# Kernel optimization log

Hardware: AMD Instinct MI355X
Metric: run time of the kernel (lower is better)

Reference implementation:

```python
import jax, jax.numpy as jnp
import numpy as np

N, E = 50000, 800000          # nodes, edges (self-loops added in reference)
IN_C, HID, OUT_C = 512, 128, 40
K, H = 4, 8                   # n_layers, heads
C = HID // H                  # per-head channels = 16
L = K + 1                     # with_initial_residual=True -> K+1 convs
NEG_SLOPE = 0.2               # PyG GATConv default leaky_relu slope


def setup_inputs():
    key = jax.random.key(0)
    ks = jax.random.split(key, 12)
    s = 0.05
    x = jax.random.normal(ks[0], (N, IN_C), jnp.float32)
    edge_index = jax.random.randint(ks[1], (2, E), 0, N, dtype=jnp.int32)
    fc0_w = jax.random.normal(ks[2], (IN_C, HID), jnp.float32) * s
    fc0_b = jax.random.normal(ks[3], (HID,), jnp.float32) * s
    lin_w = jax.random.normal(ks[4], (L, HID, HID), jnp.float32) * s      # GATConv lin (bias=False)
    att_src = jax.random.normal(ks[5], (L, H, C), jnp.float32) * s
    att_dst = jax.random.normal(ks[6], (L, H, C), jnp.float32) * s
    conv_bias = jax.random.normal(ks[7], (L, HID), jnp.float32) * s
    alphas = jnp.zeros((L,), jnp.float32).at[0].set(1.0)                  # init_alphas: t[0]=1
    fc1_w = jax.random.normal(ks[8], (HID, OUT_C), jnp.float32) * s
    fc1_b = jax.random.normal(ks[9], (OUT_C,), jnp.float32) * s
    return {"x": x, "edge_index": edge_index, "fc0_w": fc0_w, "fc0_b": fc0_b,
            "lin_w": lin_w, "att_src": att_src, "att_dst": att_dst,
            "conv_bias": conv_bias, "alphas": alphas, "fc1_w": fc1_w, "fc1_b": fc1_b}


def _gat_conv(h, src, dst, lin_w, a_src_w, a_dst_w, bias):
    # PyG GATConv (eval mode): linear -> edgewise attention -> segment softmax -> scatter-sum
    hp = (h @ lin_w).reshape(N, H, C)                 # [N,H,C]
    a_src = jnp.einsum('nhc,hc->nh', hp, a_src_w)     # [N,H]
    a_dst = jnp.einsum('nhc,hc->nh', hp, a_dst_w)
    e = jax.nn.leaky_relu(a_src[src] + a_dst[dst], NEG_SLOPE)   # [E+N,H]
    emax = jax.ops.segment_max(e, dst, num_segments=N)          # per-dst, per-head max
    e = jnp.exp(e - emax[dst])
    denom = jax.ops.segment_sum(e, dst, num_segments=N)
    alpha = e / (denom[dst] + 1e-16)                            # segment softmax
    msg = hp[src] * alpha[:, :, None]                           # [E+N,H,C]
    out = jax.ops.segment_sum(msg, dst, num_segments=N)         # [N,H,C]
    return out.reshape(N, H * C) + bias


def reference(x, edge_index, fc0_w, fc0_b, lin_w, att_src, att_dst, conv_bias, alphas, fc1_w, fc1_b):
    # forward_clenshawRes, eval mode (dropout = identity, batchNorm=False)
    loops = jnp.arange(N, dtype=edge_index.dtype)
    src = jnp.concatenate([edge_index[0], loops])   # add self-loops (PyG default)
    dst = jnp.concatenate([edge_index[1], loops])
    h0 = x @ fc0_w + fc0_b                          # fcs[0]
    last = jnp.zeros_like(h0)
    second_last = jnp.zeros_like(h0)
    for i in range(L):
        hcur = jax.nn.elu(_gat_conv(last, src, dst, lin_w[i], att_src[i], att_dst[i], conv_bias[i]))
        hcur = 2.0 * hcur - second_last + alphas[L - 1 - i] * h0   # alphas[-(i+1)]
        second_last, last = last, hcur
    out = last @ fc1_w + fc1_b                      # fcs[-1]
    return jax.nn.log_softmax(out, axis=1)
```

## Files before the change

### kernel.cpp

```cpp
#include <hip/hip_runtime.h>
#include <math.h>

#define NN      50000
#define E_CNT   800000
#define IN_C    512
#define HID     128
#define OUT_C   40
#define NHEAD   8
#define CPH     16
#define NLAYER  5
#define NEG     0.2f
#define CAP     64
#define NCOL    144

typedef __attribute__((ext_vector_type(8))) short bf16x8;
typedef __attribute__((ext_vector_type(4))) float f32x4;

__device__ __forceinline__ float lrelu(float x) { return x > 0.f ? x : NEG * x; }
__device__ __forceinline__ float eluf(float x)  { return x > 0.f ? x : expm1f(x); }

__device__ __forceinline__ float bf2f(unsigned short u) {
    union { unsigned int a; float f; } v; v.a = ((unsigned int)u) << 16;
    return v.f;
}
__device__ __forceinline__ float2 bf2f2(unsigned int u) {
    union { unsigned int a; float f; } lo, hi;
    lo.a = u << 16; hi.a = u & 0xffff0000u;
    return make_float2(lo.f, hi.f);
}
__device__ __forceinline__ unsigned short f2bf(float f) {
    union { float f; unsigned int u; } v; v.f = f;
    return (unsigned short)((v.u + 0x7fffu + ((v.u >> 16) & 1u)) >> 16);
}
__device__ __forceinline__ unsigned int pack2(float a, float b) {
    return ((unsigned int)f2bf(b) << 16) | f2bf(a);
}

__device__ __forceinline__ void gl2lds16(const void* g, void* l) {
    __builtin_amdgcn_global_load_lds(
        (const __attribute__((address_space(1))) unsigned int*)g,
        (__attribute__((address_space(3))) unsigned int*)l, 16, 0, 0);
}

__global__ __launch_bounds__(256) void k_wt(const float* __restrict__ w,
                                            unsigned short* __restrict__ wt, int K, int opitch) {
    __shared__ float t[32][33];
    const float* ws = w + (size_t)blockIdx.z * K * HID;
    unsigned short* wd = wt + (size_t)blockIdx.z * opitch;
    int k0 = blockIdx.x * 32, n0 = blockIdx.y * 32;
    int tx = threadIdx.x & 31, ty = threadIdx.x >> 5;
    for (int r = ty; r < 32; r += 8) t[r][tx] = ws[(size_t)(k0 + r) * HID + n0 + tx];
    __syncthreads();
    for (int r = ty; r < 32; r += 8) wd[(size_t)(n0 + r) * K + k0 + tx] = f2bf(t[tx][r]);
}

__global__ void k_watt(const float* __restrict__ linw, const float* __restrict__ attS,
                       const float* __restrict__ attD, unsigned short* __restrict__ wt2) {
    int i = blockIdx.x * blockDim.x + threadIdx.x;
    if (i >= 4 * 16 * HID) return;
    int l = i >> 11, r = (i >> 7) & 15, k = i & 127;
    int h = r & 7, isD = r >> 3;
    const float* W = linw + (size_t)(l + 1) * HID * HID;
    const float* av = (isD ? attD : attS) + (size_t)(l + 1) * NHEAD * CPH + h * CPH;
    float s = 0.f;
#pragma unroll
    for (int c = 0; c < CPH; ++c) s += W[(size_t)k * HID + h * CPH + c] * av[c];
    wt2[(size_t)l * NCOL * HID + (size_t)(128 + r) * HID + k] = f2bf(s);
}

template<int K, int A_F32, int NT, int EPI>
__global__ __launch_bounds__(256) void k_mgemm(const void* __restrict__ aptr,
                                               const unsigned short* __restrict__ wt,
                                               const float* __restrict__ bias,
                                               const float* __restrict__ cb0,
                                               const float* __restrict__ alphas,
                                               unsigned short* __restrict__ out_b,
                                               unsigned short* __restrict__ out_h0,
                                               float* __restrict__ aSo,
                                               float* __restrict__ aDo) {
    __shared__ unsigned short As[64 * 32];
    __shared__ unsigned short Bs[NT * 16 * 32];
    const int tid  = threadIdx.x;
    const int w    = tid >> 6, lane = tid & 63;
    const int fr   = lane & 15, fq = lane >> 4;
    const int row0 = blockIdx.x * 64;
    const int rowb = row0 + w * 16;
    const int rs = lane >> 2;
    const int ko = (lane & 3) * 8;
    f32x4 acc[NT] = {};

    for (int k0 = 0; k0 < K; k0 += 32) {
        if (A_F32) {
            int row = tid >> 2, kb = (tid & 3) * 8;
            int grow = row0 + row; if (grow >= NN) grow = NN - 1;
            const float* s = (const float*)aptr + (size_t)grow * K + k0 + kb;
            float4 v0 = *(const float4*)s, v1 = *(const float4*)(s + 4);
            union { bf16x8 v; unsigned int u[4]; } pk;
            pk.u[0] = pack2(v0.x, v0.y); pk.u[1] = pack2(v0.z, v0.w);
            pk.u[2] = pack2(v1.x, v1.y); pk.u[3] = pack2(v1.z, v1.w);
            *(bf16x8*)&As[row * 32 + kb] = pk.v;
            for (int j = w; j < NT; j += 4)
                gl2lds16(wt + (size_t)(j * 16 + rs) * K + k0 + ko, &Bs[j * 16 * 32]);
        } else {
            for (int c = w; c < 4 + NT; c += 4) {
                if (c < 4) {
                    int grow = row0 + c * 16 + rs; if (grow >= NN) grow = NN - 1;
                    gl2lds16((const unsigned short*)aptr + (size_t)grow * K + k0 + ko,
                             &As[c * 16 * 32]);
                } else {
                    int j = c - 4;
                    gl2lds16(wt + (size_t)(j * 16 + rs) * K + k0 + ko, &Bs[j * 16 * 32]);
                }
            }
        }
        __syncthreads();
        bf16x8 af = *(const bf16x8*)&As[(w * 16 + fr) * 32 + fq * 8];
#pragma unroll
        for (int t = 0; t < NT; ++t) {
            bf16x8 bfr = *(const bf16x8*)&Bs[(t * 16 + fr) * 32 + fq * 8];
            acc[t] = __builtin_amdgcn_mfma_f32_16x16x32_bf16(af, bfr, acc[t], 0, 0, 0);
        }
        __syncthreads();
    }

    const int cl = lane & 15, rq = (lane >> 4) * 4;
    const float a4 = (EPI == 2) ? alphas[NLAYER - 1] : 0.f;
#pragma unroll
    for (int t = 0; t < 8; ++t) {
        int col = t * 16 + cl;
        float bcol = (EPI == 2) ? bias[col] : 0.f;
        float ecol = (EPI == 2) ? 2.f * eluf(cb0[col]) : 0.f;
#pragma unroll
        for (int rg = 0; rg < 4; ++rg) {
            int row = rowb + rq + rg;
            if (row < NN) {
                if (EPI == 0) {
                    out_b[(size_t)row * HID + col] = f2bf(acc[t][rg]);
                } else {
                    float h0v = acc[t][rg] + bcol;
                    out_h0[(size_t)row * HID + col] = f2bf(h0v);
                    out_b[(size_t)row * HID + col]  = f2bf(ecol + a4 * h0v);
                }
            }
        }
    }
    if (NT == 9) {
#pragma unroll
        for (int rg = 0; rg < 4; ++rg) {
            int row = rowb + rq + rg;
            if (row < NN) {
                float v = acc[8][rg];
                if (cl < 8) aSo[(size_t)row * NHEAD + cl] = v;
                else        aDo[(size_t)row * NHEAD + (cl - 8)] = v;
            }
        }
    }
}

__global__ void k_hist(const int* __restrict__ dst, int* __restrict__ deg) {
    int e = blockIdx.x * blockDim.x + threadIdx.x;
    if (e < E_CNT) atomicAdd(&deg[dst[e]], 1);
}

__global__ __launch_bounds__(1024) void k_part(const int* __restrict__ deg, int* __restrict__ part) {
    int i = blockIdx.x * 1024 + threadIdx.x;
    int v = (i < NN) ? deg[i] : 0;
    for (int off = 32; off; off >>= 1) v += __shfl_down(v, off);
    __shared__ int ws[16];
    if ((threadIdx.x & 63) == 0) ws[threadIdx.x >> 6] = v;
    __syncthreads();
    if (threadIdx.x < 16) {
        int t = ws[threadIdx.x];
        for (int off = 8; off; off >>= 1) t += __shfl_down(t, off);
        if (threadIdx.x == 0) part[blockIdx.x] = t;
    }
}

__global__ void k_scanpart(int* __restrict__ part, int* __restrict__ rowstart, int nb) {
    int t = threadIdx.x;
    int v = (t < nb) ? part[t] : 0;
    int x = v;
    for (int off = 1; off < 64; off <<= 1) { int u = __shfl_up(x, off); if (t >= off) x += u; }
    if (t < nb) part[t] = x - v;
    if (t == nb - 1) rowstart[NN] = x;
}

__global__ __launch_bounds__(1024) void k_scanblk(const int* __restrict__ deg,
                                                  const int* __restrict__ partx,
                                                  int* __restrict__ rowstart,
                                                  int* __restrict__ cursor) {
    int b = blockIdx.x, t = threadIdx.x, i = b * 1024 + t;
    int v = (i < NN) ? deg[i] : 0;
    int x = v;
    for (int off = 1; off < 64; off <<= 1) { int u = __shfl_up(x, off); if ((t & 63) >= off) x += u; }
    __shared__ int ws[16];
    if ((t & 63) == 63) ws[t >> 6] = x;
    __syncthreads();
    if (t < 64) {
        int wv = (t < 16) ? ws[t] : 0;
        for (int off = 1; off < 16; off <<= 1) { int u = __shfl_up(wv, off); if (t >= off) wv += u; }
        if (t < 16) ws[t] = wv;
    }
    __syncthreads();
    int waveoff = (t >= 64) ? ws[(t >> 6) - 1] : 0;
    int excl = x - v + waveoff + partx[b];
    if (i < NN) { rowstart[i] = excl; cursor[i] = excl; }
}

__global__ void k_scatter(const int* __restrict__ src, const int* __restrict__ dst,
                          int* __restrict__ cursor, int* __restrict__ csr) {
    int e = blockIdx.x * blockDim.x + threadIdx.x;
    if (e < E_CNT) {
        int p = atomicAdd(&cursor[dst[e]], 1);
        csr[p] = src[e];
    }
}

__global__ __launch_bounds__(256) void k_agg(
    const unsigned short* __restrict__ hpb, const float* __restrict__ aS, const float* __restrict__ aD,
    const int* __restrict__ rowstart, const int* __restrict__ csr,
    const float* __restrict__ bias, const unsigned short* __restrict__ h0b,
    const unsigned short* __restrict__ slb, const float* __restrict__ alphas, int aidx, int sl_zero,
    unsigned int* __restrict__ outb) {
    __shared__ int   slds[4][CAP];
    __shared__ float wlds[4][CAP][NHEAD];
    const int wave = threadIdx.x >> 6;
    const int lane = threadIdx.x & 63;
    const int n    = blockIdx.x * 4 + wave;
    const int rsb  = rowstart[n];
    const int deg  = rowstart[n + 1] - rsb;
    const int cnt  = deg < CAP ? deg : CAP;

    for (int j = lane; j < cnt; j += 64) slds[wave][j] = csr[rsb + j];
    __syncthreads();

    const int h    = lane & 7;
    const int slot = lane >> 3;
    const float adst = aD[n * NHEAD + h];

    float den = 0.f;
#pragma unroll
    for (int t = 0; t < 8; ++t) {
        int j = slot + t * 8;
        if (j < cnt) {
            int s = slds[wave][j];
            float wv = __expf(lrelu(aS[s * NHEAD + h] + adst));
            wlds[wave][j][h] = wv;
            den += wv;
        }
    }
    for (int j = CAP + slot; j < deg; j += 8)
        den += __expf(lrelu(aS[csr[rsb + j] * NHEAD + h] + adst));
#pragma unroll
    for (int off = 8; off < 64; off <<= 1) den += __shfl_xor(den, off);
    const float w0 = __expf(lrelu(aS[n * NHEAD + h] + adst));
    den += w0;
    const float dinv = 1.f / (den + 1e-16f);
    __syncthreads();

    const int l    = lane & 31;
    const int half = lane >> 5;
    const int hh   = l >> 2;
    const float w0h = __shfl(w0, hh);
    const float dih = __shfl(dinv, hh);
    const float adh = __shfl(adst, hh);

    float a0 = 0.f, a1 = 0.f, a2 = 0.f, a3 = 0.f;
    if (half == 0) {
        uint2 u = *(const uint2*)(hpb + (size_t)n * HID + 4 * l);
        float2 p = bf2f2(u.x), q = bf2f2(u.y);
        a0 = w0h * p.x; a1 = w0h * p.y; a2 = w0h * q.x; a3 = w0h * q.y;
    }
    if (deg <= CAP) {
#pragma unroll 4
        for (int j = half; j < deg; j += 2) {
            int s = slds[wave][j];
            float wv = wlds[wave][j][hh];
            uint2 u = *(const uint2*)(hpb + (size_t)s * HID + 4 * l);
            float2 p = bf2f2(u.x), q = bf2f2(u.y);
            a0 += wv * p.x; a1 += wv * p.y; a2 += wv * q.x; a3 += wv * q.y;
        }
    } else {
        for (int j = half; j < deg; j += 2) {
            int s; float wv;
            if (j < CAP) { s = slds[wave][j]; wv = wlds[wave][j][hh]; }
            else { s = csr[rsb + j]; wv = __expf(lrelu(aS[s * NHEAD + hh] + adh)); }
            uint2 u = *(const uint2*)(hpb + (size_t)s * HID + 4 * l);
            float2 p = bf2f2(u.x), q = bf2f2(u.y);
            a0 += wv * p.x; a1 += wv * p.y; a2 += wv * q.x; a3 += wv * q.y;
        }
    }
    a0 += __shfl_xor(a0, 32); a1 += __shfl_xor(a1, 32);
    a2 += __shfl_xor(a2, 32); a3 += __shfl_xor(a3, 32);

    if (half == 0) {
        float4 bv = ((const float4*)bias)[l];
        float g0 = eluf(a0 * dih + bv.x);
        float g1 = eluf(a1 * dih + bv.y);
        float g2 = eluf(a2 * dih + bv.z);
        float g3 = eluf(a3 * dih + bv.w);
        const float ac = alphas[aidx];
        float s0 = 0.f, s1 = 0.f, s2 = 0.f, s3 = 0.f;
        if (!sl_zero) {
            uint2 su = *(const uint2*)(slb + (size_t)n * HID + 4 * l);
            float2 p = bf2f2(su.x), q = bf2f2(su.y);
            s0 = p.x; s1 = p.y; s2 = q.x; s3 = q.y;
        }
        float hx0 = 0.f, hx1 = 0.f, hx2 = 0.f, hx3 = 0.f;
        if (ac != 0.f) {
            uint2 hu = *(const uint2*)(h0b + (size_t)n * HID + 4 * l);
            float2 p = bf2f2(hu.x), q = bf2f2(hu.y);
            hx0 = p.x; hx1 = p.y; hx2 = q.x; hx3 = q.y;
        }
        float o0 = 2.f * g0 - s0 + ac * hx0;
        float o1 = 2.f * g1 - s1 + ac * hx1;
        float o2 = 2.f * g2 - s2 + ac * hx2;
        float o3 = 2.f * g3 - s3 + ac * hx3;
        uint2 pb; pb.x = pack2(o0, o1); pb.y = pack2(o2, o3);
        ((uint2*)outb)[(size_t)n * 32 + l] = pb;
    }
}

__global__ __launch_bounds__(64) void k_out(const unsigned short* __restrict__ t,
                                            const float* __restrict__ w,
                                            const float* __restrict__ b,
                                            float* __restrict__ out) {
    const int n = blockIdx.x;
    const int lane = threadIdx.x;
    float acc = 0.f;
    if (lane < OUT_C) {
        const unsigned short* row = t + (size_t)n * HID;
        for (int k = 0; k < HID; ++k) acc += bf2f(row[k]) * w[k * OUT_C + lane];
        acc += b[lane];
    }
    float v = (lane < OUT_C) ? acc : -INFINITY;
    for (int off = 32; off; off >>= 1) v = fmaxf(v, __shfl_down(v, off));
    float mx = __shfl(v, 0);
    float ex = (lane < OUT_C) ? __expf(acc - mx) : 0.f;
    float sv = ex;
    for (int off = 32; off; off >>= 1) sv += __shfl_down(sv, off);
    float lse = logf(__shfl(sv, 0));
    if (lane < OUT_C) out[(size_t)n * OUT_C + lane] = acc - mx - lse;
}

extern "C" void kernel_launch(void* const* d_in, const int* in_sizes, int n_in,
                              void* d_out, int out_size, void* d_ws, size_t ws_size,
                              hipStream_t stream) {
    const float* x      = (const float*)d_in[0];
    const int*   ei     = (const int*)  d_in[1];
    const float* fc0w   = (const float*)d_in[2];
    const float* fc0b   = (const float*)d_in[3];
    const float* linw   = (const float*)d_in[4];
    const float* attS   = (const float*)d_in[5];
    const float* attD   = (const float*)d_in[6];
    const float* cbias  = (const float*)d_in[7];
    const float* alphas = (const float*)d_in[8];
    const float* fc1w   = (const float*)d_in[9];
    const float* fc1b   = (const float*)d_in[10];
    float* out = (float*)d_out;

    char* p = (char*)d_ws;
    auto alloc = [&](size_t bytes) { void* q = (void*)p; p += (bytes + 255) / 256 * 256; return q; };
    const size_t NB16 = (size_t)NN * HID * 2;
    unsigned short* h0b  = (unsigned short*)alloc(NB16);
    unsigned short* Lb0  = (unsigned short*)alloc(NB16);
    unsigned short* Lb1  = (unsigned short*)alloc(NB16);
    unsigned short* Lb2  = (unsigned short*)alloc(NB16);
    unsigned short* hpb  = (unsigned short*)alloc(NB16);
    float* aSb = (float*)alloc((size_t)NN * NHEAD * 4);
    float* aDb = (float*)alloc((size_t)NN * NHEAD * 4);
    unsigned short* WT0 = (unsigned short*)alloc((size_t)HID * IN_C * 2);
    unsigned short* WT2 = (unsigned short*)alloc((size_t)4 * NCOL * HID * 2);
    int* deg      = (int*)alloc((size_t)(NN + 1) * 4);
    int* rowstart = (int*)alloc((size_t)(NN + 1) * 4);
    int* part     = (int*)alloc(64 * 4);
    int* csr      = (int*)alloc((size_t)E_CNT * 4);
    int* cursor   = deg;

    const int* esrc = ei;
    const int* edst = ei + E_CNT;
    const int NB = (NN + 1023) / 1024;

    hipMemsetAsync(deg, 0, (size_t)NN * 4, stream);
    k_hist<<<(E_CNT + 255) / 256, 256, 0, stream>>>(edst, deg);
    k_part<<<NB, 1024, 0, stream>>>(deg, part);
    k_scanpart<<<1, 64, 0, stream>>>(part, rowstart, NB);
    k_scanblk<<<NB, 1024, 0, stream>>>(deg, part, rowstart, cursor);
    k_scatter<<<(E_CNT + 255) / 256, 256, 0, stream>>>(esrc, edst, cursor, csr);

    {
        dim3 g0(IN_C / 32, HID / 32, 1);
        k_wt<<<g0, 256, 0, stream>>>(fc0w, WT0, IN_C, HID * IN_C);
        dim3 gl(HID / 32, HID / 32, 4);
        k_wt<<<gl, 256, 0, stream>>>(linw + (size_t)HID * HID, WT2, HID, NCOL * HID);
        k_watt<<<(4 * 16 * HID + 255) / 256, 256, 0, stream>>>(linw, attS, attD, WT2);
    }

    const int GB = (NN + 63) / 64;
    k_mgemm<IN_C, 1, 8, 2><<<GB, 256, 0, stream>>>(x, WT0, fc0b, cbias, alphas,
                                                   Lb0, h0b, nullptr, nullptr);

    unsigned short* last = Lb0; unsigned short* sl = Lb1; unsigned short* nxt = Lb2;
    for (int i = 1; i < NLAYER; ++i) {
        k_mgemm<HID, 0, 9, 0><<<GB, 256, 0, stream>>>(last, WT2 + (size_t)(i - 1) * NCOL * HID,
                                                      nullptr, nullptr, nullptr, hpb, nullptr, aSb, aDb);
        k_agg<<<NN / 4, 256, 0, stream>>>(hpb, aSb, aDb, rowstart, csr,
                                          cbias + i * HID, h0b, sl, alphas, NLAYER - 1 - i, (i == 1) ? 1 : 0,
                                          (unsigned int*)nxt);
        unsigned short* tmp = sl; sl = last; last = nxt; nxt = tmp;
    }

    k_out<<<NN, 64, 0, stream>>>(last, fc1w, fc1b, out);
}
```

Baseline: 595.7 us.

## Use MFMA for output projection and widen aggregation gathers to 16-byte loads

The final fc1 projection plus log-softmax, previously one 64-thread block per node doing a scalar dot-product loop, becomes a tiled bf16 MFMA GEMM over 64-row blocks with a padded, pre-transposed weight and an in-register log-softmax. Separately, the aggregation kernel now gathers 8 bf16 channels per lane with 16-byte loads, processing four neighbours in parallel per wave instead of two, then reduces across quarter-waves. This trades more accumulator registers and an extra shuffle stage for fewer, wider memory transactions and far fewer tiny output blocks.

```diff
diff --git a/kernel.cpp b/kernel.cpp
--- a/kernel.cpp
+++ b/kernel.cpp
@@ -66,6 +66,13 @@
 #pragma unroll
     for (int c = 0; c < CPH; ++c) s += W[(size_t)k * HID + h * CPH + c] * av[c];
     wt2[(size_t)l * NCOL * HID + (size_t)(128 + r) * HID + k] = f2bf(s);
+}
+
+__global__ void k_wout(const float* __restrict__ w, unsigned short* __restrict__ wt1) {
+    int i = blockIdx.x * blockDim.x + threadIdx.x;
+    if (i >= 48 * HID) return;
+    int r = i >> 7, k = i & 127;
+    wt1[i] = (r < OUT_C) ? f2bf(w[(size_t)k * OUT_C + r]) : (unsigned short)0;
 }
 
 template<int K, int A_F32, int NT, int EPI>
@@ -157,6 +164,80 @@
     }
 }
 
+__global__ __launch_bounds__(256) void k_out(const unsigned short* __restrict__ ab,
+                                             const unsigned short* __restrict__ wt1,
+                                             const float* __restrict__ b,
+                                             float* __restrict__ out) {
+    __shared__ unsigned short As[64 * 32];
+    __shared__ unsigned short Bs[48 * 32];
+    const int tid  = threadIdx.x;
+    const int w    = tid >> 6, lane = tid & 63;
+    const int fr   = lane & 15, fq = lane >> 4;
+    const int row0 = blockIdx.x * 64;
+    const int rowb = row0 + w * 16;
+    const int rs = lane >> 2;
+    const int ko = (lane & 3) * 8;
+    f32x4 acc[3] = {};
+
+    for (int k0 = 0; k0 < HID; k0 += 32) {
+        for (int c = w; c < 7; c += 4) {
+            if (c < 4) {
+                int grow = row0 + c * 16 + rs; if (grow >= NN) grow = NN - 1;
+                gl2lds16(ab + (size_t)grow * HID + k0 + ko, &As[c * 16 * 32]);
+            } else {
+                int j = c - 4;
+                gl2lds16(wt1 + (size_t)(j * 16 + rs) * HID + k0 + ko, &Bs[j * 16 * 32]);
+            }
+        }
+        __syncthreads();
+        bf16x8 af = *(const bf16x8*)&As[(w * 16 + fr) * 32 + fq * 8];
+#pragma unroll
+        for (int t = 0; t < 3; ++t) {
+            bf16x8 bfr = *(const bf16x8*)&Bs[(t * 16 + fr) * 32 + fq * 8];
+            acc[t] = __builtin_amdgcn_mfma_f32_16x16x32_bf16(af, bfr, acc[t], 0, 0, 0);
+        }
+        __syncthreads();
+    }
+
+    const int cl = lane & 15, rq = (lane >> 4) * 4;
+    float b3[3];
+#pragma unroll
+    for (int t = 0; t < 3; ++t) {
+        int col = t * 16 + cl;
+        b3[t] = (col < OUT_C) ? b[col] : 0.f;
+    }
+#pragma unroll
+    for (int rg = 0; rg < 4; ++rg) {
+        int row = rowb + rq + rg;
+        float v[3];
+        float mx = -1e30f;
+#pragma unroll
+        for (int t = 0; t < 3; ++t) {
+            int col = t * 16 + cl;
+            v[t] = acc[t][rg] + b3[t];
+            if (col < OUT_C) mx = fmaxf(mx, v[t]);
+        }
+#pragma unroll
+        for (int off = 1; off < 16; off <<= 1) mx = fmaxf(mx, __shfl_xor(mx, off));
+        float sum = 0.f;
+#pragma unroll
+        for (int t = 0; t < 3; ++t) {
+            int col = t * 16 + cl;
+            if (col < OUT_C) sum += __expf(v[t] - mx);
+        }
+#pragma unroll
+        for (int off = 1; off < 16; off <<= 1) sum += __shfl_xor(sum, off);
+        float lse = mx + logf(sum);
+        if (row < NN) {
+#pragma unroll
+            for (int t = 0; t < 3; ++t) {
+                int col = t * 16 + cl;
+                if (col < OUT_C) out[(size_t)row * OUT_C + col] = v[t] - lse;
+            }
+        }
+    }
+}
+
 __global__ void k_hist(const int* __restrict__ dst, int* __restrict__ deg) {
     int e = blockIdx.x * blockDim.x + threadIdx.x;
     if (e < E_CNT) atomicAdd(&deg[dst[e]], 1);
@@ -258,89 +339,77 @@
     const float dinv = 1.f / (den + 1e-16f);
     __syncthreads();
 
-    const int l    = lane & 31;
-    const int half = lane >> 5;
-    const int hh   = l >> 2;
+    const int l  = lane & 15;
+    const int q  = lane >> 4;
+    const int hh = l >> 1;
     const float w0h = __shfl(w0, hh);
     const float dih = __shfl(dinv, hh);
     const float adh = __shfl(adst, hh);
 
-    float a0 = 0.f, a1 = 0.f, a2 = 0.f, a3 = 0.f;
-    if (half == 0) {
-        uint2 u = *(const uint2*)(hpb + (size_t)n * HID + 4 * l);
-        float2 p = bf2f2(u.x), q = bf2f2(u.y);
-        a0 = w0h * p.x; a1 = w0h * p.y; a2 = w0h * q.x; a3 = w0h * q.y;
+    float c0 = 0.f, c1 = 0.f, c2 = 0.f, c3 = 0.f, c4 = 0.f, c5 = 0.f, c6 = 0.f, c7 = 0.f;
+    if (q == 0) {
+        uint4 u = *(const uint4*)(hpb + (size_t)n * HID + 8 * l);
+        float2 p0 = bf2f2(u.x), p1 = bf2f2(u.y), p2 = bf2f2(u.z), p3 = bf2f2(u.w);
+        c0 = w0h * p0.x; c1 = w0h * p0.y; c2 = w0h * p1.x; c3 = w0h * p1.y;
+        c4 = w0h * p2.x; c5 = w0h * p2.y; c6 = w0h * p3.x; c7 = w0h * p3.y;
     }
     if (deg <= CAP) {
-#pragma unroll 4
-        for (int j = half; j < deg; j += 2) {
+#pragma unroll 2
+        for (int j = q; j < deg; j += 4) {
             int s = slds[wave][j];
             float wv = wlds[wave][j][hh];
-            uint2 u = *(const uint2*)(hpb + (size_t)s * HID + 4 * l);
-            float2 p = bf2f2(u.x), q = bf2f2(u.y);
-            a0 += wv * p.x; a1 += wv * p.y; a2 += wv * q.x; a3 += wv * q.y;
+            uint4 u = *(const uint4*)(hpb + (size_t)s * HID + 8 * l);
+            float2 p0 = bf2f2(u.x), p1 = bf2f2(u.y), p2 = bf2f2(u.z), p3 = bf2f2(u.w);
+            c0 += wv * p0.x; c1 += wv * p0.y; c2 += wv * p1.x; c3 += wv * p1.y;
+            c4 += wv * p2.x; c5 += wv * p2.y; c6 += wv * p3.x; c7 += wv * p3.y;
         }
     } else {
-        for (int j = half; j < deg; j += 2) {
+        for (int j = q; j < deg; j += 4) {
             int s; float wv;
             if (j < CAP) { s = slds[wave][j]; wv = wlds[wave][j][hh]; }
             else { s = csr[rsb + j]; wv = __expf(lrelu(aS[s * NHEAD + hh] + adh)); }
-            uint2 u = *(const uint2*)(hpb + (size_t)s * HID + 4 * l);
-            float2 p = bf2f2(u.x), q = bf2f2(u.y);
-            a0 += wv * p.x; a1 += wv * p.y; a2 += wv * q.x; a3 += wv * q.y;
-        }
-    }
-    a0 += __shfl_xor(a0, 32); a1 += __shfl_xor(a1, 32);
-    a2 += __shfl_xor(a2, 32); a3 += __shfl_xor(a3, 32);
-
-    if (half == 0) {
-        float4 bv = ((const float4*)bias)[l];
-        float g0 = eluf(a0 * dih + bv.x);
-        float g1 = eluf(a1 * dih + bv.y);
-        float g2 = eluf(a2 * dih + bv.z);
-        float g3 = eluf(a3 * dih + bv.w);
+            uint4 u = *(const uint4*)(hpb + (size_t)s * HID + 8 * l);
+            float2 p0 = bf2f2(u.x), p1 = bf2f2(u.y), p2 = bf2f2(u.z), p3 = bf2f2(u.w);
+            c0 += wv * p0.x; c1 += wv * p0.y; c2 += wv * p1.x; c3 += wv * p1.y;
+            c4 += wv * p2.x; c5 += wv * p2.y; c6 += wv * p3.x; c7 += wv * p3.y;
+        }
+    }
+    c0 += __shfl_xor(c0, 16); c1 += __shfl_xor(c1, 16); c2 += __shfl_xor(c2, 16); c3 += __shfl_xor(c3, 16);
+    c4 += __shfl_xor(c4, 16); c5 += __shfl_xor(c5, 16); c6 += __shfl_xor(c6, 16); c7 += __shfl_xor(c7, 16);
+    c0 += __shfl_xor(c0, 32); c1 += __shfl_xor(c1, 32); c2 += __shfl_xor(c2, 32); c3 += __shfl_xor(c3, 32);
+    c4 += __shfl_xor(c4, 32); c5 += __shfl_xor(c5, 32); c6 += __shfl_xor(c6, 32); c7 += __shfl_xor(c7, 32);
+
+    if (q == 0) {
+        float4 bv0 = ((const float4*)bias)[2 * l];
+        float4 bv1 = ((const float4*)bias)[2 * l + 1];
+        float g0 = eluf(c0 * dih + bv0.x);
+        float g1 = eluf(c1 * dih + bv0.y);
+        float g2 = eluf(c2 * dih + bv0.z);
+        float g3 = eluf(c3 * dih + bv0.w);
+        float g4 = eluf(c4 * dih + bv1.x);
+        float g5 = eluf(c5 * dih + bv1.y);
+        float g6 = eluf(c6 * dih + bv1.z);
+        float g7 = eluf(c7 * dih + bv1.w);
         const float ac = alphas[aidx];
-        float s0 = 0.f, s1 = 0.f, s2 = 0.f, s3 = 0.f;
+        float s0 = 0.f, s1 = 0.f, s2 = 0.f, s3 = 0.f, s4 = 0.f, s5 = 0.f, s6 = 0.f, s7 = 0.f;
         if (!sl_zero) {
-            uint2 su = *(const uint2*)(slb + (size_t)n * HID + 4 * l);
-            float2 p = bf2f2(su.x), q = bf2f2(su.y);
-            s0 = p.x; s1 = p.y; s2 = q.x; s3 = q.y;
-        }
-        float hx0 = 0.f, hx1 = 0.f, hx2 = 0.f, hx3 = 0.f;
+            uint4 su = *(const uint4*)(slb + (size_t)n * HID + 8 * l);
+            float2 p0 = bf2f2(su.x), p1 = bf2f2(su.y), p2 = bf2f2(su.z), p3 = bf2f2(su.w);
+            s0 = p0.x; s1 = p0.y; s2 = p1.x; s3 = p1.y; s4 = p2.x; s5 = p2.y; s6 = p3.x; s7 = p3.y;
+        }
+        float hx0 = 0.f, hx1 = 0.f, hx2 = 0.f, hx3 = 0.f, hx4 = 0.f, hx5 = 0.f, hx6 = 0.f, hx7 = 0.f;
         if (ac != 0.f) {
-            uint2 hu = *(const uint2*)(h0b + (size_t)n * HID + 4 * l);
-            float2 p = bf2f2(hu.x), q = bf2f2(hu.y);
-            hx0 = p.x; hx1 = p.y; hx2 = q.x; hx3 = q.y;
-        }
-        float o0 = 2.f * g0 - s0 + ac * hx0;
-        float o1 = 2.f * g1 - s1 + ac * hx1;
-        float o2 = 2.f * g2 - s2 + ac * hx2;
-        float o3 = 2.f * g3 - s3 + ac * hx3;
-        uint2 pb; pb.x = pack2(o0, o1); pb.y = pack2(o2, o3);
-        ((uint2*)outb)[(size_t)n * 32 + l] = pb;
-    }
-}
-
-__global__ __launch_bounds__(64) void k_out(const unsigned short* __restrict__ t,
-                                            const float* __restrict__ w,
-                                            const float* __restrict__ b,
-                                            float* __restrict__ out) {
-    const int n = blockIdx.x;
-    const int lane = threadIdx.x;
-    float acc = 0.f;
-    if (lane < OUT_C) {
-        const unsigned short* row = t + (size_t)n * HID;
-        for (int k = 0; k < HID; ++k) acc += bf2f(row[k]) * w[k * OUT_C + lane];
-        acc += b[lane];
-    }
-    float v = (lane < OUT_C) ? acc : -INFINITY;
-    for (int off = 32; off; off >>= 1) v = fmaxf(v, __shfl_down(v, off));
-    float mx = __shfl(v, 0);
-    float ex = (lane < OUT_C) ? __expf(acc - mx) : 0.f;
-    float sv = ex;
-    for (int off = 32; off; off >>= 1) sv += __shfl_down(sv, off);
-    float lse = logf(__shfl(sv, 0));
-    if (lane < OUT_C) out[(size_t)n * OUT_C + lane] = acc - mx - lse;
+            uint4 hu = *(const uint4*)(h0b + (size_t)n * HID + 8 * l);
+            float2 p0 = bf2f2(hu.x), p1 = bf2f2(hu.y), p2 = bf2f2(hu.z), p3 = bf2f2(hu.w);
+            hx0 = p0.x; hx1 = p0.y; hx2 = p1.x; hx3 = p1.y; hx4 = p2.x; hx5 = p2.y; hx6 = p3.x; hx7 = p3.y;
+        }
+        uint4 pb;
+        pb.x = pack2(2.f * g0 - s0 + ac * hx0, 2.f * g1 - s1 + ac * hx1);
+        pb.y = pack2(2.f * g2 - s2 + ac * hx2, 2.f * g3 - s3 + ac * hx3);
+        pb.z = pack2(2.f * g4 - s4 + ac * hx4, 2.f * g5 - s5 + ac * hx5);
+        pb.w = pack2(2.f * g6 - s6 + ac * hx6, 2.f * g7 - s7 + ac * hx7);
+        ((uint4*)outb)[(size_t)n * 16 + l] = pb;
+    }
 }
 
 extern "C" void kernel_launch(void* const* d_in, const int* in_sizes, int n_in,
@@ -371,6 +440,7 @@
     float* aDb = (float*)alloc((size_t)NN * NHEAD * 4);
     unsigned short* WT0 = (unsigned short*)alloc((size_t)HID * IN_C * 2);
     unsigned short* WT2 = (unsigned short*)alloc((size_t)4 * NCOL * HID * 2);
+    unsigned short* WT1 = (unsigned short*)alloc((size_t)48 * HID * 2);
     int* deg      = (int*)alloc((size_t)(NN + 1) * 4);
     int* rowstart = (int*)alloc((size_t)(NN + 1) * 4);
     int* part     = (int*)alloc(64 * 4);
@@ -394,6 +464,7 @@
         dim3 gl(HID / 32, HID / 32, 4);
         k_wt<<<gl, 256, 0, stream>>>(linw + (size_t)HID * HID, WT2, HID, NCOL * HID);
         k_watt<<<(4 * 16 * HID + 255) / 256, 256, 0, stream>>>(linw, attS, attD, WT2);
+        k_wout<<<(48 * HID + 255) / 256, 256, 0, stream>>>(fc1w, WT1);
     }
 
     const int GB = (NN + 63) / 64;
@@ -410,5 +481,5 @@
         unsigned short* tmp = sl; sl = last; last = nxt; nxt = tmp;
     }
 
-    k_out<<<NN, 64, 0, stream>>>(last, fc1w, fc1b, out);
-}
+    k_out<<<GB, 256, 0, stream>>>(last, WT1, fc1b, out);
+}
```

Result: faster. 544.2 us (-8.6%).
